# Kernel tuning notes

Hardware: AMD Instinct MI355X
Metric: run time of the kernel (lower is better)

## Reference

```python
import jax, jax.numpy as jnp
import numpy as np

D_MODEL = 64
N_HEADS = 4
HEAD_DIM = D_MODEL // N_HEADS  # 16
D_FF = 4 * D_MODEL  # 256
LN_EPS = 1e-5


def _layer_norm(x, g, b):
    mu = jnp.mean(x, axis=-1, keepdims=True)
    var = jnp.var(x, axis=-1, keepdims=True)
    return (x - mu) * jax.lax.rsqrt(var + LN_EPS) * g + b


def setup_inputs() -> dict:
    key = jax.random.key(0)
    ks = jax.random.split(key, 16)
    B, S = 4, 2048
    s = 0.05
    return {
        "x": jax.random.normal(ks[0], (B, S, D_MODEL), dtype=jnp.float32),
        # per-head projection weights (stacked over the head axis)
        "wq": jax.random.normal(ks[1], (N_HEADS, D_MODEL, HEAD_DIM), dtype=jnp.float32) * s,
        "bq": jax.random.normal(ks[2], (N_HEADS, HEAD_DIM), dtype=jnp.float32) * s,
        "wk": jax.random.normal(ks[3], (N_HEADS, D_MODEL, HEAD_DIM), dtype=jnp.float32) * s,
        "bk": jax.random.normal(ks[4], (N_HEADS, HEAD_DIM), dtype=jnp.float32) * s,
        "wv": jax.random.normal(ks[5], (N_HEADS, D_MODEL, HEAD_DIM), dtype=jnp.float32) * s,
        "bv": jax.random.normal(ks[6], (N_HEADS, HEAD_DIM), dtype=jnp.float32) * s,
        "wo": jax.random.normal(ks[7], (D_MODEL, D_MODEL), dtype=jnp.float32) * s,
        "bo": jax.random.normal(ks[8], (D_MODEL,), dtype=jnp.float32) * s,
        "ln1_g": jnp.ones((D_MODEL,), dtype=jnp.float32),
        "ln1_b": jnp.zeros((D_MODEL,), dtype=jnp.float32),
        "w1": jax.random.normal(ks[9], (D_MODEL, D_FF), dtype=jnp.float32) * s,
        "b1": jax.random.normal(ks[10], (D_FF,), dtype=jnp.float32) * s,
        "w2": jax.random.normal(ks[11], (D_FF, D_MODEL), dtype=jnp.float32) * s,
        "b2": jax.random.normal(ks[12], (D_MODEL,), dtype=jnp.float32) * s,
        "ln2_g": jnp.ones((D_MODEL,), dtype=jnp.float32),
        "ln2_b": jnp.zeros((D_MODEL,), dtype=jnp.float32),
    }


def reference(x, wq, bq, wk, bk, wv, bv, wo, bo, ln1_g, ln1_b, w1, b1, w2, b2, ln2_g, ln2_b):
    B, S, _ = x.shape
    # per-head projections, vectorized over the head axis
    Q = jnp.einsum('bsd,hdk->bhsk', x, wq) + bq[None, :, None, :]
    K = jnp.einsum('bsd,hdk->bhsk', x, wk) + bk[None, :, None, :]
    V = jnp.einsum('bsd,hdk->bhsk', x, wv) + bv[None, :, None, :]
    # scaled causal attention (mask materialized as in the original)
    scores = jnp.einsum('bhsk,bhtk->bhst', Q, K) / jnp.sqrt(jnp.float32(HEAD_DIM))
    causal = jnp.tril(jnp.ones((S, S), dtype=bool))  # keep lower triangle
    scores = jnp.where(causal, scores, -jnp.inf)
    attn = jax.nn.softmax(scores, axis=-1)
    A = jnp.einsum('bhst,bhtk->bhsk', attn, V)
    # concat heads -> [B, S, D]
    A = A.transpose(0, 2, 1, 3).reshape(B, S, D_MODEL)
    out = A @ wo + bo
    out = out + x
    out = _layer_norm(out, ln1_g, ln1_b)
    ff = jnp.maximum(out @ w1 + b1, 0.0) @ w2 + b2  # dropout is identity in eval
    out = _layer_norm(ff + out, ln2_g, ln2_b)
    return out
```

## Files before the change

kernel.cpp:

```cpp
#include <hip/hip_runtime.h>

#define DEVFN __device__ __forceinline__

constexpr int B = 4, S = 2048, H = 4, DH = 16, D = 64, F = 256;
constexpr int T = B * S;
constexpr int PAIRS = B * H;
constexpr int CPP = 72;
constexpr int NZ = PAIRS * CPP;
constexpr int PSTRIDE = 1280;
constexpr float LOG2E = 1.44269504f;

typedef __attribute__((ext_vector_type(8))) short s16x8;
typedef __attribute__((ext_vector_type(16))) float f32x16;
typedef __attribute__((ext_vector_type(4))) float f32x4;

DEVFN float wave_sum(float v) {
#pragma unroll
    for (int mask = 32; mask >= 1; mask >>= 1)
        v += __shfl_xor(v, mask, 64);
    return v;
}

DEVFN float bf2f(unsigned short u) { return __uint_as_float((unsigned)u << 16); }
DEVFN unsigned short f2bf(float f) {
    unsigned b = __float_as_uint(f);
    return (unsigned short)((b + 0x8000u) >> 16);
}
DEVFN unsigned pack_bf2(float lo, float hi) {
    unsigned a = __float_as_uint(lo), b = __float_as_uint(hi);
    return ((a + 0x8000u) >> 16) | ((b + 0x8000u) & 0xffff0000u);
}
DEVFN unsigned cvtpk(float lo, float hi) {
    unsigned r;
    asm("v_cvt_pk_bf16_f32 %0, %1, %2" : "=v"(r) : "v"(lo), "v"(hi));
    return r;
}
DEVFN void plswap(unsigned& a, unsigned& b) {
#if __has_builtin(__builtin_amdgcn_permlane32_swap)
    typedef unsigned uv2 __attribute__((ext_vector_type(2)));
    uv2 r = __builtin_amdgcn_permlane32_swap(a, b, false, false);
    a = r[0]; b = r[1];
#else
    asm volatile("v_permlane32_swap_b32 %0, %1" : "+v"(a), "+v"(b));
#endif
}

__global__ __launch_bounds__(256) void k_qkv(
    const float* __restrict__ x,
    const float* __restrict__ wq, const float* __restrict__ bq,
    const float* __restrict__ wk, const float* __restrict__ bk,
    const float* __restrict__ wv, const float* __restrict__ bv,
    const float* __restrict__ wo, const float* __restrict__ w1,
    const float* __restrict__ w2,
    unsigned short* __restrict__ Qb, unsigned short* __restrict__ Kb,
    unsigned short* __restrict__ Vtg,
    unsigned* __restrict__ wob, unsigned* __restrict__ w1b,
    unsigned* __restrict__ w2b)
{
    __shared__ float xst[64][36];
    int tid = threadIdx.x;
    int t0 = blockIdx.x * 32;

    int token = tid >> 3, dseg = tid & 7;
    float4 xa = *(const float4*)(x + (size_t)(t0 + token) * D + dseg * 8);
    float4 xb = *(const float4*)(x + (size_t)(t0 + token) * D + dseg * 8 + 4);

    if (blockIdx.x < 16) {
        int bi = blockIdx.x;
        if (tid < 128) {
            int i = bi * 128 + tid;
            int jt = i >> 9, ks = (i >> 8) & 1, l = (i >> 2) & 63, ee = 2 * (i & 3);
            int j = 16 * jt + (l & 15);
            int k = 32 * ks + 8 * (l >> 4) + ee;
            wob[i] = pack_bf2(wo[k * D + j], wo[(k + 1) * D + j]);
        }
#pragma unroll
        for (int e = 0; e < 2; ++e) {
            int i = bi * 512 + e * 256 + tid;
            int ft = i >> 9, ks = (i >> 8) & 1, l = (i >> 2) & 63, ee = 2 * (i & 3);
            int f = 16 * ft + (l & 15);
            int k = 32 * ks + 8 * (l >> 4) + ee;
            w1b[i] = pack_bf2(w1[k * F + f], w1[(k + 1) * F + f]);
        }
#pragma unroll
        for (int e = 0; e < 2; ++e) {
            int i = bi * 512 + e * 256 + tid;
            int jt = i >> 11, ks = (i >> 8) & 7, l = (i >> 2) & 63, ee = 2 * (i & 3);
            int j = 16 * jt + (l & 15);
            int k = 32 * ks + 8 * (l >> 4) + ee;
            w2b[i] = pack_bf2(w2[k * D + j], w2[(k + 1) * D + j]);
        }
    }

    xst[dseg * 8 + 0][token] = xa.x;
    xst[dseg * 8 + 1][token] = xa.y;
    xst[dseg * 8 + 2][token] = xa.z;
    xst[dseg * 8 + 3][token] = xa.w;
    xst[dseg * 8 + 4][token] = xb.x;
    xst[dseg * 8 + 5][token] = xb.y;
    xst[dseg * 8 + 6][token] = xb.z;
    xst[dseg * 8 + 7][token] = xb.w;
    __syncthreads();

    int j = tid & 63, g = tid >> 6;
    int h = j >> 4, k = j & 15;
    int wbase = h * (D * DH) + k;

    float qa[8], ka[8], va[8];
#pragma unroll
    for (int i = 0; i < 8; ++i) { qa[i] = bq[j]; ka[i] = bk[j]; va[i] = bv[j]; }

#pragma unroll 4
    for (int d = 0; d < D; ++d) {
        float wqv = wq[wbase + d * DH];
        float wkv = wk[wbase + d * DH];
        float wvv = wv[wbase + d * DH];
        float4 xv0 = *(const float4*)&xst[d][g * 8];
        float4 xv1 = *(const float4*)&xst[d][g * 8 + 4];
        float xe[8] = { xv0.x, xv0.y, xv0.z, xv0.w, xv1.x, xv1.y, xv1.z, xv1.w };
#pragma unroll
        for (int i = 0; i < 8; ++i) {
            qa[i] = fmaf(xe[i], wqv, qa[i]);
            ka[i] = fmaf(xe[i], wkv, ka[i]);
            va[i] = fmaf(xe[i], wvv, va[i]);
        }
    }
    int b = t0 >> 11;
    int pair = b * H + h;
    unsigned short vv[8];
#pragma unroll
    for (int i = 0; i < 8; ++i) {
        int t = t0 + g * 8 + i;
        int s = t & (S - 1);
        int off = (pair * S + s) * DH + k;
        Qb[off] = f2bf(qa[i] * (0.25f * LOG2E));
        Kb[off] = f2bf(ka[i]);
        vv[i] = f2bf(va[i]);
    }
    int s0 = (t0 & (S - 1)) + g * 8;
    uint4 pk;
    pk.x = (unsigned)vv[0] | ((unsigned)vv[1] << 16);
    pk.y = (unsigned)vv[2] | ((unsigned)vv[3] << 16);
    pk.z = (unsigned)vv[4] | ((unsigned)vv[5] << 16);
    pk.w = (unsigned)vv[6] | ((unsigned)vv[7] << 16);
    *(uint4*)(Vtg + (size_t)(pair * DH + k) * S + s0) = pk;
}

__global__ __launch_bounds__(256) void k_attn_part(
    const unsigned short* __restrict__ Qb, const unsigned short* __restrict__ Kb,
    const unsigned short* __restrict__ Vtg, float* __restrict__ P)
{
    __shared__ unsigned short Kt[256][16];
    __shared__ unsigned short Vt[16][264];

    int tid = threadIdx.x, lane = tid & 63, w = tid >> 6;

    int bid0 = blockIdx.x;
    int z = (bid0 & 7) * 144 + (bid0 >> 3);
    int pair = z / CPP;
    int rem = z - pair * CPP;
    int qb = 0, cum = 0;
    while (cum + (qb >> 1) + 1 <= rem) { cum += (qb >> 1) + 1; ++qb; }
    int kc = rem - cum;
    int kbase = kc << 8;
    int qbase = qb << 7;

    {
        const uint4* src = (const uint4*)(Kb + (size_t)(pair * S + kbase + tid) * DH);
        uint4 lo = src[0], hi = src[1];
        *(uint4*)&Kt[tid][(tid & 1) * 8] = lo;
        *(uint4*)&Kt[tid][((tid & 1) ^ 1) * 8] = hi;
        int r = tid >> 4, cc = tid & 15;
        const uint4* vs = (const uint4*)(Vtg + (size_t)(pair * DH + r) * S + kbase + cc * 16);
        uint4 v0 = vs[0], v1 = vs[1];
        *(uint4*)&Vt[r][cc * 16] = v0;
        *(uint4*)&Vt[r][cc * 16 + 8] = v1;
    }
    __syncthreads();

    int qn = lane & 31, g = lane >> 5;
    int q0w = qbase + w * 32;
    int qg = q0w + qn;
    int vrow = lane & 15;

    s16x8 qf = *(const s16x8*)(Qb + (size_t)(pair * S + qg) * DH + g * 8);

    f32x16 czero;
#pragma unroll
    for (int i = 0; i < 16; ++i) czero[i] = 0.f;
    f32x16 acc = czero;
    float mrun = -1e30f, lsum = 0.f;

    int nt = ((q0w + 31 - kbase) >> 5) + 1;
    if (nt > 8) nt = 8;

    int krow0 = qn;
    s16x8 kf = *(const s16x8*)&Kt[krow0][(g ^ (krow0 & 1)) * 8];

    for (int t = 0; t < nt; ++t) {
        int kl = t * 32;
        s16x8 vf0 = *(const s16x8*)&Vt[vrow][kl + g * 8];
        s16x8 vf1 = *(const s16x8*)&Vt[vrow][kl + 16 + g * 8];
        int tn = (t + 1 < nt) ? (t + 1) : t;
        int krown = tn * 32 + qn;
        s16x8 kfn = *(const s16x8*)&Kt[krown][(g ^ (krown & 1)) * 8];

        f32x16 sc = __builtin_amdgcn_mfma_f32_32x32x16_bf16(kf, qf, czero, 0, 0, 0);
        if (t == nt - 1) {
            int qml = qg - (kbase + kl);
#pragma unroll
            for (int r = 0; r < 16; ++r) {
                int m = (r & 3) + 8 * (r >> 2) + 4 * g;
                sc[r] = (m <= qml) ? sc[r] : -1e30f;
            }
        }
        float t0a = fmaxf(fmaxf(sc[0], sc[1]), sc[2]);
        float t1a = fmaxf(fmaxf(sc[3], sc[4]), sc[5]);
        float t2a = fmaxf(fmaxf(sc[6], sc[7]), sc[8]);
        float t3a = fmaxf(fmaxf(sc[9], sc[10]), sc[11]);
        float t4a = fmaxf(fmaxf(sc[12], sc[13]), sc[14]);
        float tm = fmaxf(fmaxf(fmaxf(t0a, t1a), fmaxf(t2a, t3a)),
                         fmaxf(t4a, sc[15]));
        tm = fmaxf(tm, __shfl_xor(tm, 32, 64));
        float mnew = fmaxf(mrun, tm);
        float scale = exp2f(mrun - mnew);
        mrun = mnew;
        float p[16];
        float ts0 = 0.f, ts1 = 0.f, ts2 = 0.f, ts3 = 0.f;
#pragma unroll
        for (int r = 0; r < 16; r += 4) {
            p[r]     = exp2f(sc[r] - mnew);     ts0 += p[r];
            p[r + 1] = exp2f(sc[r + 1] - mnew); ts1 += p[r + 1];
            p[r + 2] = exp2f(sc[r + 2] - mnew); ts2 += p[r + 2];
            p[r + 3] = exp2f(sc[r + 3] - mnew); ts3 += p[r + 3];
        }
        float ts = (ts0 + ts1) + (ts2 + ts3);
        ts += __shfl_xor(ts, 32, 64);
        lsum = fmaf(lsum, scale, ts);
#pragma unroll
        for (int r = 0; r < 8; ++r) acc[r] *= scale;

        unsigned a0 = cvtpk(p[0],  p[1]);
        unsigned a1 = cvtpk(p[2],  p[3]);
        unsigned a2 = cvtpk(p[4],  p[5]);
        unsigned a3 = cvtpk(p[6],  p[7]);
        unsigned b0 = cvtpk(p[8],  p[9]);
        unsigned b1 = cvtpk(p[10], p[11]);
        unsigned b2 = cvtpk(p[12], p[13]);
        unsigned b3 = cvtpk(p[14], p[15]);
        plswap(a0, a2);
        plswap(a1, a3);
        plswap(b0, b2);
        plswap(b1, b3);
        union UU { unsigned u[4]; s16x8 v; };
        UU pf0, pf1;
        pf0.u[0] = a0; pf0.u[1] = a1; pf0.u[2] = a2; pf0.u[3] = a3;
        pf1.u[0] = b0; pf1.u[1] = b1; pf1.u[2] = b2; pf1.u[3] = b3;

        acc = __builtin_amdgcn_mfma_f32_32x32x16_bf16(vf0, pf0.v, acc, 0, 0, 0);
        acc = __builtin_amdgcn_mfma_f32_32x32x16_bf16(vf1, pf1.v, acc, 0, 0, 0);
        kf = kfn;
    }

    float* base = P + (size_t)z * PSTRIDE;
    if (lane < 32) {
        base[w * 32 + qn] = mrun;
        base[128 + w * 32 + qn] = lsum;
    }
    uint2 cA, cB;
    cA.x = pack_bf2(acc[0], acc[1]); cA.y = pack_bf2(acc[2], acc[3]);
    cB.x = pack_bf2(acc[4], acc[5]); cB.y = pack_bf2(acc[6], acc[7]);
    unsigned short* pa = (unsigned short*)(base + 256);
    *(uint2*)&pa[(w * 32 + qn) * 16 + 4 * g] = cA;
    *(uint2*)&pa[(w * 32 + qn) * 16 + 8 + 4 * g] = cB;
}

__global__ __launch_bounds__(256) void k_post(
    const float* __restrict__ P, const float* __restrict__ x,
    const unsigned* __restrict__ wob, const float* __restrict__ bo,
    const float* __restrict__ g1, const float* __restrict__ bb1,
    const unsigned* __restrict__ w1b, const float* __restrict__ b1,
    const unsigned* __restrict__ w2b, const float* __restrict__ b2,
    const float* __restrict__ g2, const float* __restrict__ bb2,
    float* __restrict__ out)
{
    __shared__ unsigned short Asb[16][72];
    __shared__ float Os[16][68];
    __shared__ float R1s[16][68];
    __shared__ unsigned short R1sb[16][72];
    __shared__ unsigned short Hhb[16][264];

    int tid = threadIdx.x, lane = tid & 63, w = tid >> 6;
    int t0 = blockIdx.x * 16;
    int b = t0 >> 11;
    int sbase = t0 & (S - 1);
    int qb = sbase >> 7;
    int nc = (qb >> 1) + 1;
    int cum = 0;
#pragma unroll
    for (int i = 0; i < 16; ++i) cum += (i < qb) ? ((i >> 1) + 1) : 0;

    {
        int token = tid >> 4, sub = tid & 15;
        int h = sub >> 2, dq = sub & 3;
        int pair = b * H + h;
        int q = (sbase & 127) + token;
        const float* base0 = P + ((size_t)pair * CPP + cum) * PSTRIDE;

        float mv[8], sv[8]; uint2 uv[8];
#pragma unroll
        for (int c = 0; c < 8; ++c) {
            int cc = (c < nc) ? c : (nc - 1);
            const float* bc = base0 + cc * PSTRIDE;
            float m_ = bc[q];
            float s_ = bc[128 + q];
            uint2 u_ = *(const uint2*)((const unsigned*)(bc + 256) + q * 8 + dq * 2);
            bool valid = (c < nc);
            mv[c] = valid ? m_ : -1e30f;
            sv[c] = valid ? s_ : 0.f;
            uv[c].x = valid ? u_.x : 0u;
            uv[c].y = valid ? u_.y : 0u;
        }
        float M = fmaxf(fmaxf(fmaxf(mv[0], mv[1]), fmaxf(mv[2], mv[3])),
                        fmaxf(fmaxf(mv[4], mv[5]), fmaxf(mv[6], mv[7])));
        float Sm = 0.f, a0 = 0.f, a1 = 0.f, a2 = 0.f, a3 = 0.f;
#pragma unroll
        for (int c = 0; c < 8; ++c) {
            float e = exp2f(mv[c] - M);
            Sm = fmaf(sv[c], e, Sm);
            a0 = fmaf(__uint_as_float(uv[c].x << 16), e, a0);
            a1 = fmaf(__uint_as_float(uv[c].x & 0xffff0000u), e, a1);
            a2 = fmaf(__uint_as_float(uv[c].y << 16), e, a2);
            a3 = fmaf(__uint_as_float(uv[c].y & 0xffff0000u), e, a3);
        }
        float inv = 1.f / Sm;
        uint2 o;
        o.x = cvtpk(a0 * inv, a1 * inv);
        o.y = cvtpk(a2 * inv, a3 * inv);
        *(uint2*)&Asb[token][16 * h + 4 * dq] = o;
    }
    __syncthreads();

    {
        f32x4 c = {0.f, 0.f, 0.f, 0.f};
#pragma unroll
        for (int ks = 0; ks < 2; ++ks) {
            s16x8 af = *(const s16x8*)&Asb[lane & 15][32 * ks + 8 * (lane >> 4)];
            s16x8 bf = *(const s16x8*)(wob + (((w * 2) + ks) * 64 + lane) * 4);
            c = __builtin_amdgcn_mfma_f32_16x16x32_bf16(af, bf, c, 0, 0, 0);
        }
        int j = 16 * w + (lane & 15);
        int q4 = lane >> 4;
        float boj = bo[j];
#pragma unroll
        for (int r = 0; r < 4; ++r) {
            int tk = q4 * 4 + r;
            Os[tk][j] = c[r] + boj + x[(size_t)(t0 + tk) * D + j];
        }
    }
    __syncthreads();

    {
        int j = lane;
        float gj = g1[j], bj = bb1[j];
#pragma unroll
        for (int i = 0; i < 4; ++i) {
            int tk = w * 4 + i;
            float o = Os[tk][j];
            float mu = wave_sum(o) * (1.f / 64.f);
            float dif = o - mu;
            float var = wave_sum(dif * dif) * (1.f / 64.f);
            float r1 = dif * rsqrtf(var + 1e-5f) * gj + bj;
            R1s[tk][j] = r1;
            R1sb[tk][j] = f2bf(r1);
        }
    }
    __syncthreads();

    {
        int q4 = lane >> 4;
#pragma unroll
        for (int t = 0; t < 4; ++t) {
            int ft = w * 4 + t;
            f32x4 c = {0.f, 0.f, 0.f, 0.f};
#pragma unroll
            for (int ks = 0; ks < 2; ++ks) {
                s16x8 af = *(const s16x8*)&R1sb[lane & 15][32 * ks + 8 * (lane >> 4)];
                s16x8 bf = *(const s16x8*)(w1b + (((ft * 2) + ks) * 64 + lane) * 4);
                c = __builtin_amdgcn_mfma_f32_16x16x32_bf16(af, bf, c, 0, 0, 0);
            }
            int f = 16 * ft + (lane & 15);
            float b1f = b1[f];
#pragma unroll
            for (int r = 0; r < 4; ++r)
                Hhb[q4 * 4 + r][f] = f2bf(fmaxf(c[r] + b1f, 0.f));
        }
    }
    __syncthreads();

    {
        f32x4 c = {0.f, 0.f, 0.f, 0.f};
#pragma unroll
        for (int ks = 0; ks < 8; ++ks) {
            s16x8 af = *(const s16x8*)&Hhb[lane & 15][32 * ks + 8 * (lane >> 4)];
            s16x8 bf = *(const s16x8*)(w2b + (((w * 8) + ks) * 64 + lane) * 4);
            c = __builtin_amdgcn_mfma_f32_16x16x32_bf16(af, bf, c, 0, 0, 0);
        }
        int j = 16 * w + (lane & 15);
        int q4 = lane >> 4;
        float b2j = b2[j];
#pragma unroll
        for (int r = 0; r < 4; ++r) {
            int tk = q4 * 4 + r;
            Os[tk][j] = c[r] + b2j + R1s[tk][j];
        }
    }
    __syncthreads();

    {
        int j = lane;
        float gj = g2[j], bj = bb2[j];
#pragma unroll
        for (int i = 0; i < 4; ++i) {
            int tk = w * 4 + i;
            float y = Os[tk][j];
            float mu = wave_sum(y) * (1.f / 64.f);
            float dif = y - mu;
            float var = wave_sum(dif * dif) * (1.f / 64.f);
            out[(size_t)(t0 + tk) * D + j] = dif * rsqrtf(var + 1e-5f) * gj + bj;
        }
    }
}

extern "C" void kernel_launch(void* const* d_in, const int* in_sizes, int n_in,
                              void* d_out, int out_size, void* d_ws, size_t ws_size,
                              hipStream_t stream)
{
    const float* x   = (const float*)d_in[0];
    const float* wq  = (const float*)d_in[1];
    const float* bq  = (const float*)d_in[2];
    const float* wk  = (const float*)d_in[3];
    const float* bk  = (const float*)d_in[4];
    const float* wv  = (const float*)d_in[5];
    const float* bv  = (const float*)d_in[6];
    const float* wo  = (const float*)d_in[7];
    const float* bo  = (const float*)d_in[8];
    const float* g1  = (const float*)d_in[9];
    const float* be1 = (const float*)d_in[10];
    const float* w1  = (const float*)d_in[11];
    const float* b1  = (const float*)d_in[12];
    const float* w2  = (const float*)d_in[13];
    const float* b2  = (const float*)d_in[14];
    const float* g2  = (const float*)d_in[15];
    const float* be2 = (const float*)d_in[16];

    char* base = (char*)d_ws;
    unsigned short* Qb  = (unsigned short*)base;
    unsigned short* Kb  = (unsigned short*)(base + (1u << 20));
    unsigned short* Vtg = (unsigned short*)(base + (2u << 20));
    float*          P   = (float*)(base + (3u << 20));
    unsigned*       wob = (unsigned*)(base + (9u << 20));
    unsigned*       w1b = (unsigned*)(base + (9u << 20) + 0x10000);
    unsigned*       w2b = (unsigned*)(base + (9u << 20) + 0x20000);

    k_qkv      <<<T / 32, 256, 0, stream>>>(x, wq, bq, wk, bk, wv, bv,
                                            wo, w1, w2, Qb, Kb, Vtg,
                                            wob, w1b, w2b);
    k_attn_part<<<NZ, 256, 0, stream>>>(Qb, Kb, Vtg, P);
    k_post     <<<T / 16, 256, 0, stream>>>(P, x, wob, bo, g1, be1,
                                            w1b, b1, w2b, b2, g2, be2,
                                            (float*)d_out);
}
```

Baseline: 45.18 us.

## Compute QKV projection with bf16 MFMA instead of scalar FMA

```diff
diff --git a/kernel.cpp b/kernel.cpp
--- a/kernel.cpp
+++ b/kernel.cpp
@@ -57,13 +57,35 @@
     unsigned* __restrict__ wob, unsigned* __restrict__ w1b,
     unsigned* __restrict__ w2b)
 {
-    __shared__ float xst[64][36];
-    int tid = threadIdx.x;
+    __shared__ __align__(16) unsigned short xfr[2][2][64][8];
+    __shared__ __align__(16) unsigned short wfr[12][2][64][8];
+
+    int tid = threadIdx.x, lane = tid & 63, w = tid >> 6;
     int t0 = blockIdx.x * 32;
-
-    int token = tid >> 3, dseg = tid & 7;
-    float4 xa = *(const float4*)(x + (size_t)(t0 + token) * D + dseg * 8);
-    float4 xb = *(const float4*)(x + (size_t)(t0 + token) * D + dseg * 8 + 4);
+    int b = t0 >> 11;
+    int sbase = t0 & (S - 1);
+
+#pragma unroll
+    for (int e = 0; e < 4; ++e) {
+        int i = e * 256 + tid;
+        int tt = i >> 9, ks = (i >> 8) & 1, l = (i >> 2) & 63, ee = 2 * (i & 3);
+        int token = 16 * tt + (l & 15);
+        int kk = 32 * ks + 8 * (l >> 4) + ee;
+        float2 xv = *(const float2*)(x + (size_t)(t0 + token) * D + kk);
+        *(unsigned*)&xfr[tt][ks][l][ee] = pack_bf2(xv.x, xv.y);
+    }
+#pragma unroll
+    for (int e = 0; e < 24; ++e) {
+        int i = e * 256 + tid;
+        int combo = i >> 9, ks = (i >> 8) & 1, l = (i >> 2) & 63, ee = 2 * (i & 3);
+        int m = combo >> 2, jt = combo & 3;
+        int j15 = l & 15;
+        int kk = 32 * ks + 8 * (l >> 4) + ee;
+        const float* wsrc = (m == 0) ? wq : (m == 1) ? wk : wv;
+        float a = wsrc[jt * 1024 + kk * 16 + j15];
+        float c = wsrc[jt * 1024 + (kk + 1) * 16 + j15];
+        *(unsigned*)&wfr[combo][ks][l][ee] = pack_bf2(a, c);
+    }
 
     if (blockIdx.x < 16) {
         int bi = blockIdx.x;
@@ -91,59 +113,45 @@
             w2b[i] = pack_bf2(w2[k * D + j], w2[(k + 1) * D + j]);
         }
     }
-
-    xst[dseg * 8 + 0][token] = xa.x;
-    xst[dseg * 8 + 1][token] = xa.y;
-    xst[dseg * 8 + 2][token] = xa.z;
-    xst[dseg * 8 + 3][token] = xa.w;
-    xst[dseg * 8 + 4][token] = xb.x;
-    xst[dseg * 8 + 5][token] = xb.y;
-    xst[dseg * 8 + 6][token] = xb.z;
-    xst[dseg * 8 + 7][token] = xb.w;
-    __syncthreads();
-
-    int j = tid & 63, g = tid >> 6;
-    int h = j >> 4, k = j & 15;
-    int wbase = h * (D * DH) + k;
-
-    float qa[8], ka[8], va[8];
-#pragma unroll
-    for (int i = 0; i < 8; ++i) { qa[i] = bq[j]; ka[i] = bk[j]; va[i] = bv[j]; }
-
-#pragma unroll 4
-    for (int d = 0; d < D; ++d) {
-        float wqv = wq[wbase + d * DH];
-        float wkv = wk[wbase + d * DH];
-        float wvv = wv[wbase + d * DH];
-        float4 xv0 = *(const float4*)&xst[d][g * 8];
-        float4 xv1 = *(const float4*)&xst[d][g * 8 + 4];
-        float xe[8] = { xv0.x, xv0.y, xv0.z, xv0.w, xv1.x, xv1.y, xv1.z, xv1.w };
-#pragma unroll
-        for (int i = 0; i < 8; ++i) {
-            qa[i] = fmaf(xe[i], wqv, qa[i]);
-            ka[i] = fmaf(xe[i], wkv, ka[i]);
-            va[i] = fmaf(xe[i], wvv, va[i]);
-        }
-    }
-    int b = t0 >> 11;
-    int pair = b * H + h;
-    unsigned short vv[8];
-#pragma unroll
-    for (int i = 0; i < 8; ++i) {
-        int t = t0 + g * 8 + i;
-        int s = t & (S - 1);
-        int off = (pair * S + s) * DH + k;
-        Qb[off] = f2bf(qa[i] * (0.25f * LOG2E));
-        Kb[off] = f2bf(ka[i]);
-        vv[i] = f2bf(va[i]);
-    }
-    int s0 = (t0 & (S - 1)) + g * 8;
-    uint4 pk;
-    pk.x = (unsigned)vv[0] | ((unsigned)vv[1] << 16);
-    pk.y = (unsigned)vv[2] | ((unsigned)vv[3] << 16);
-    pk.z = (unsigned)vv[4] | ((unsigned)vv[5] << 16);
-    pk.w = (unsigned)vv[6] | ((unsigned)vv[7] << 16);
-    *(uint4*)(Vtg + (size_t)(pair * DH + k) * S + s0) = pk;
+    __syncthreads();
+
+    int j15 = lane & 15, q4 = lane >> 4;
+#pragma unroll
+    for (int t3 = 0; t3 < 3; ++t3) {
+        int combo = w * 3 + t3;
+        int m = combo >> 2, jt = combo & 3;
+        int j = 16 * jt + j15;
+        int pair = b * H + jt;
+#pragma unroll
+        for (int tt = 0; tt < 2; ++tt) {
+            f32x4 c = {0.f, 0.f, 0.f, 0.f};
+#pragma unroll
+            for (int ks = 0; ks < 2; ++ks) {
+                s16x8 af = *(const s16x8*)&xfr[tt][ks][lane][0];
+                s16x8 bf = *(const s16x8*)&wfr[combo][ks][lane][0];
+                c = __builtin_amdgcn_mfma_f32_16x16x32_bf16(af, bf, c, 0, 0, 0);
+            }
+            int s0 = sbase + 16 * tt + 4 * q4;
+            if (m == 0) {
+                float bj = bq[j];
+#pragma unroll
+                for (int r = 0; r < 4; ++r)
+                    Qb[((size_t)pair * S + s0 + r) * DH + j15] =
+                        f2bf((c[r] + bj) * (0.25f * LOG2E));
+            } else if (m == 1) {
+                float bj = bk[j];
+#pragma unroll
+                for (int r = 0; r < 4; ++r)
+                    Kb[((size_t)pair * S + s0 + r) * DH + j15] = f2bf(c[r] + bj);
+            } else {
+                float bj = bv[j];
+                uint2 o;
+                o.x = pack_bf2(c[0] + bj, c[1] + bj);
+                o.y = pack_bf2(c[2] + bj, c[3] + bj);
+                *(uint2*)(Vtg + ((size_t)pair * DH + j15) * S + s0) = o;
+            }
+        }
+    }
 }
 
 __global__ __launch_bounds__(256) void k_attn_part(
```

Measured after the change: 38.94 us. 13.8% less time.
